# Optimization experiments

Measured on AMD Instinct MI355X. Metric: run time of the kernel, lower is better.

## Reference

```python
import jax, jax.numpy as jnp
import numpy as np

B, T, M = 4, 512, 77
H, D = 10, 64            # num_heads, latent_dim
LAT = H * D              # 640 = latent_dim * num_heads
E, TOPK, FFN = 8, 2, 256 # experts, top-k, 4*latent_dim
TED = 512                # time_embed_dim
NDS = 4                  # num_datasets


def layernorm(x, g, b, eps=1e-5):
    m = x.mean(-1, keepdims=True)
    v = ((x - m) ** 2).mean(-1, keepdims=True)
    return (x - m) * jax.lax.rsqrt(v + eps) * g + b


def moe_ffn(x, wg, w1, b1, w2, b2):
    # x: (N, D). Top-k gated mixture of expert FFNs (tutel-style, fp32 gate,
    # no capacity truncation in this reference).
    logits = x.astype(jnp.float32) @ wg.astype(jnp.float32)        # (N, E)
    scores = jax.nn.softmax(logits, -1)
    vals, idx = jax.lax.top_k(scores, TOPK)                        # (N, k)
    comb = (jax.nn.one_hot(idx, E, dtype=scores.dtype) * vals[..., None]).sum(1)  # (N, E)
    h = jax.nn.gelu(jnp.einsum('nd,edf->nef', x, w1) + b1)         # (N, E, F)
    y = jnp.einsum('nef,efd->ned', h, w2) + b2                     # (N, E, D)
    return jnp.einsum('ne,ned->nd', comb.astype(x.dtype), y)


def setup_inputs() -> dict:
    key = jax.random.key(0)
    ks = jax.random.split(key, 24)
    s = 0.02
    f32 = jnp.float32
    return {
        'x': jax.random.normal(ks[0], (B, T, LAT), f32),
        'emb': jax.random.normal(ks[1], (B, T, TED), f32),
        'src_mask': jax.random.randint(ks[2], (B, T), 0, 2).astype(jnp.int32),
        'motion_length': jax.random.randint(ks[3], (B,), 1, T).astype(jnp.int32),
        'num_intervals': 1,
        'text_cond': jnp.ones((B, 1), f32),
        'text_word_out': jax.random.normal(ks[4], (B, M, LAT), f32),
        'norm_g': jnp.ones((LAT,), f32), 'norm_b': jnp.zeros((LAT,), f32),
        'moe_emb': jax.random.normal(ks[5], (1, T, H, D), f32) * s,
        'm_wg': jax.random.normal(ks[6], (D, E), f32) * s,
        'm_w1': jax.random.normal(ks[7], (E, D, FFN), f32) * s,
        'm_b1': jnp.zeros((E, FFN), f32),
        'm_w2': jax.random.normal(ks[8], (E, FFN, D), f32) * s,
        'm_b2': jnp.zeros((E, D), f32),
        'm_proj_w': jax.random.normal(ks[9], (D, 5 * D), f32) * s,
        'm_proj_b': jnp.zeros((5 * D,), f32),
        'key_motion_scale': jnp.ones((), f32),
        'sigma': jnp.asarray(100.0, f32),
        'key_dataset': jax.random.normal(ks[10], (NDS, 48, H, D), f32) * s,
        'key_dataset_scale': jnp.ones((), f32),
        'value_dataset': jax.random.normal(ks[11], (NDS, 48, H, D), f32) * s,
        'key_rotation': jax.random.normal(ks[12], (3, 16, H, D), f32) * s,
        'key_rotation_scale': jnp.ones((), f32),
        'value_rotation': jax.random.normal(ks[13], (3, 16, H, D), f32) * s,
        'normt_g': jnp.ones((LAT,), f32), 'normt_b': jnp.zeros((LAT,), f32),
        'c_wg': jax.random.normal(ks[14], (D, E), f32) * s,
        'c_w1': jax.random.normal(ks[15], (E, D, FFN), f32) * s,
        'c_b1': jnp.zeros((E, FFN), f32),
        'c_w2': jax.random.normal(ks[16], (E, FFN, D), f32) * s,
        'c_b2': jnp.zeros((E, D), f32),
        'c_proj_w': jax.random.normal(ks[17], (D, 2 * D), f32) * s,
        'c_proj_b': jnp.zeros((2 * D,), f32),
        'key_text_scale': jnp.ones((), f32),
        'st_emb_w': jax.random.normal(ks[18], (TED, 2 * LAT), f32) * s,
        'st_emb_b': jnp.zeros((2 * LAT,), f32),
        'st_norm_g': jnp.ones((LAT,), f32), 'st_norm_b': jnp.zeros((LAT,), f32),
        'st_out_w': jax.random.normal(ks[19], (LAT, LAT), f32) * s,
        'st_out_b': jnp.zeros((LAT,), f32),
    }


def reference(x, emb, src_mask, motion_length, num_intervals, text_cond, text_word_out,
              norm_g, norm_b, moe_emb, m_wg, m_w1, m_b1, m_w2, m_b2, m_proj_w, m_proj_b,
              key_motion_scale, sigma, key_dataset, key_dataset_scale, value_dataset,
              key_rotation, key_rotation_scale, value_rotation, normt_g, normt_b,
              c_wg, c_w1, c_b1, c_w2, c_b2, c_proj_w, c_proj_b, key_text_scale,
              st_emb_w, st_emb_b, st_norm_g, st_norm_b, st_out_w, st_out_b):
    b, t, _ = x.shape
    # motion MoE -> per-head q, k, v (output is 5*D; last 2 chunks are template feats, unused here)
    xh = layernorm(x, norm_g, norm_b).reshape(b, t, H, D) + moe_emb[:, :t]
    y = moe_ffn(xh.reshape(-1, D), m_wg, m_w1, m_b1, m_w2, m_b2)
    y = (jax.nn.gelu(y) @ m_proj_w + m_proj_b).reshape(b, t, H, 5 * D)
    q, k_m, v_m = y[..., :D], y[..., D:2 * D], y[..., 2 * D:3 * D]

    # text conditioning MoE -> key/value (output is 2*D)
    m = text_word_out.shape[1]
    ct = layernorm(text_word_out, normt_g, normt_b).reshape(b, m, H, D)
    cy = moe_ffn(ct.reshape(-1, D), c_wg, c_w1, c_b1, c_w2, c_b2)
    cy = (jax.nn.gelu(cy) @ c_proj_w + c_proj_b).reshape(b, m, H, 2 * D)
    k_t, v_t = cy[..., :D], cy[..., D:]

    sc = D ** -0.5
    # motion keys: Gaussian time-locality bias (sigma) + src_mask
    lg_m = jnp.einsum('bthd,bshd->bhts', q, k_m * key_motion_scale) * sc
    ti = jnp.arange(t)
    lg_m = lg_m - ((ti[:, None] - ti[None, :]).astype(x.dtype) ** 2) / (2.0 * sigma ** 2)
    lg_m = jnp.where((src_mask > 0)[:, None, None, :], lg_m, -1e9)
    # dataset / rotation learned key-value banks (dataset index 0)
    lg_d = jnp.einsum('bthd,shd->bhts', q, key_dataset[0] * key_dataset_scale) * sc
    lg_r = jnp.einsum('bthd,shd->bhts', q, key_rotation.reshape(-1, H, D) * key_rotation_scale) * sc
    # text keys, masked by text_cond
    lg_t = jnp.einsum('bthd,bmhd->bhtm', q, k_t * key_text_scale) * sc
    lg_t = jnp.where((text_cond[:, 0] > 0)[:, None, None, None], lg_t, -1e9)

    attn = jax.nn.softmax(jnp.concatenate([lg_m, lg_d, lg_r, lg_t], -1), -1)
    a_m, a_d = attn[..., :t], attn[..., t:t + 48]
    a_r, a_t = attn[..., t + 48:t + 96], attn[..., t + 96:]
    out = (jnp.einsum('bhts,bshd->bthd', a_m, v_m)
           + jnp.einsum('bhts,shd->bthd', a_d, value_dataset[0])
           + jnp.einsum('bhts,shd->bthd', a_r, value_rotation.reshape(-1, H, D))
           + jnp.einsum('bhtm,bmhd->bthd', a_t, v_t)).reshape(b, t, LAT)

    # StylizationBlock (MotionDiffuse-style) + residual
    eo = jax.nn.silu(emb) @ st_emb_w + st_emb_b            # (B,T,2*LAT)
    hh = layernorm(out, st_norm_g, st_norm_b) * (1.0 + eo[..., :LAT]) + eo[..., LAT:]
    return x + (jax.nn.silu(hh) @ st_out_w + st_out_b)
```

## Files before the change

kernel.cpp:

```cpp
#include <hip/hip_runtime.h>
#include <math.h>

#define BB 4
#define TT 512
#define MM 77
#define HH 10
#define DD 64
#define LATD 640
#define EE 8
#define FFND 256
#define NS 685
#define NCH 11
#define NROWS 20480
#define NSPLIT 4

#define NTOK_M (BB*TT*HH)
#define NTOK_T (BB*MM*HH)
#define MAXB_M 647
#define MAXB_T 103
#define PROJB_M 320
#define PROJB_T 49
#define ROUTEB_M 80
#define ROUTEB_T 13
#define ATTNB (BB*HH*8*NSPLIT)
#define GEMM1B 1280

typedef float f32x4 __attribute__((ext_vector_type(4)));
typedef __bf16 bf16x8_t __attribute__((ext_vector_type(8)));
typedef unsigned short u16x8 __attribute__((ext_vector_type(8)));

__device__ __forceinline__ float geluf(float x){
    float u = 0.7978845608028654f*(x + 0.044715f*x*x*x);
    u = fminf(fmaxf(u, -15.f), 15.f);
    float e = __expf(2.f*u);
    return 0.5f*x*(1.f + (e-1.f)/(e+1.f));
}
__device__ __forceinline__ float siluf(float x){
    return x / (1.0f + __expf(-x));
}
__device__ __forceinline__ unsigned short f2bf(float f){
    unsigned int u = __float_as_uint(f);
    u += 0x7fff + ((u >> 16) & 1);
    return (unsigned short)(u >> 16);
}
__device__ __forceinline__ uint2 pack4bf(float a, float b, float c, float d){
    uint2 r;
    r.x = (unsigned)f2bf(a) | ((unsigned)f2bf(b)<<16);
    r.y = (unsigned)f2bf(c) | ((unsigned)f2bf(d)<<16);
    return r;
}

__global__ __launch_bounds__(256) void prep_ln_kernel(
    const float* __restrict__ m_w1, unsigned short* __restrict__ w1Tm,
    const float* __restrict__ m_w2, unsigned short* __restrict__ w2Tm,
    const float* __restrict__ c_w1, unsigned short* __restrict__ w1Tt,
    const float* __restrict__ c_w2, unsigned short* __restrict__ w2Tt,
    const float* __restrict__ st_ew, unsigned short* __restrict__ stewT,
    const float* __restrict__ st_ow, unsigned short* __restrict__ stowT,
    const float* __restrict__ m_pw, unsigned short* __restrict__ mpwT,
    const float* __restrict__ c_pw, unsigned short* __restrict__ cpwT,
    const float* __restrict__ emb, unsigned short* __restrict__ embBf,
    int* __restrict__ cnt,
    const float* __restrict__ x, const float* __restrict__ ng, const float* __restrict__ nb,
    const float* __restrict__ memb, float* __restrict__ xh,
    const float* __restrict__ two, const float* __restrict__ ntg, const float* __restrict__ ntb,
    float* __restrict__ ctB)
{
    __shared__ float buf[64*65];
    const int bid = blockIdx.x, tid = threadIdx.x;
    if (bid >= 651){
        int lrow = bid - 651;
        const float* in; const float* g; const float* bb; const float* ap; float* out;
        int row;
        if (lrow < BB*TT){
            row = lrow; in = x; g = ng; bb = nb; out = xh;
            ap = memb + (size_t)(row % TT)*LATD;
        } else {
            row = lrow - BB*TT; in = two; g = ntg; bb = ntb; out = ctB;
            ap = nullptr;
        }
        float* xsr = buf;
        float* red = buf + LATD;
        const float* rp = in + (size_t)row*LATD;
        float s = 0.f;
        for (int i=tid;i<LATD;i+=256){ float v = rp[i]; xsr[i]=v; s+=v; }
        red[tid]=s; __syncthreads();
        for (int k=128;k>0;k>>=1){ if (tid<k) red[tid]+=red[tid+k]; __syncthreads(); }
        float mean = red[0]*(1.0f/LATD);
        __syncthreads();
        float vs=0.f;
        for (int i=tid;i<LATD;i+=256){ float d=xsr[i]-mean; vs+=d*d; }
        red[tid]=vs; __syncthreads();
        for (int k=128;k>0;k>>=1){ if (tid<k) red[tid]+=red[tid+k]; __syncthreads(); }
        float rstd = rsqrtf(red[0]*(1.0f/LATD)+1e-5f);
        float* op = out + (size_t)row*LATD;
        for (int i=tid;i<LATD;i+=256){
            float v = (xsr[i]-mean)*rstd*g[i] + bb[i];
            if (ap) v += ap[i];
            op[i] = v;
        }
        return;
    }
    if (bid >= 395){
        int l = bid - 395;
        if (l == 0 && tid < 16) cnt[tid] = 0;
        size_t base = (size_t)l*4096;
        #pragma unroll
        for (int p=0; p<4; ++p){
            size_t i = base + (size_t)p*1024 + tid*4;
            float4 v = *(const float4*)(emb + i);
            *(uint2*)(embBf + i) = pack4bf(siluf(v.x), siluf(v.y), siluf(v.z), siluf(v.w));
        }
        return;
    }
    float (*t)[65] = (float(*)[65])buf;
    const float* in; unsigned short* out; int R, C, z, rt, ct;
    if (bid < 32)      { int l=bid;     in=m_w1;  out=w1Tm;  R=64;  C=256;  z=l>>2; rt=0;    ct=l&3; }
    else if (bid < 64) { int l=bid-32;  in=m_w2;  out=w2Tm;  R=256; C=64;   z=l>>2; rt=l&3;  ct=0; }
    else if (bid < 96) { int l=bid-64;  in=c_w1;  out=w1Tt;  R=64;  C=256;  z=l>>2; rt=0;    ct=l&3; }
    else if (bid < 128){ int l=bid-96;  in=c_w2;  out=w2Tt;  R=256; C=64;   z=l>>2; rt=l&3;  ct=0; }
    else if (bid < 288){ int l=bid-128; in=st_ew; out=stewT; R=512; C=1280; z=0;    rt=l/20; ct=l%20; }
    else if (bid < 388){ int l=bid-288; in=st_ow; out=stowT; R=640; C=640;  z=0;    rt=l/10; ct=l%10; }
    else if (bid < 393){ int l=bid-388; in=m_pw;  out=mpwT;  R=64;  C=320;  z=0;    rt=0;    ct=l; }
    else               { int l=bid-393; in=c_pw;  out=cpwT;  R=64;  C=128;  z=0;    rt=0;    ct=l; }
    const size_t base = (size_t)z*R*C;
    const int r0 = rt*64, c0 = ct*64;
    #pragma unroll
    for (int p=0; p<16; ++p){
        int i = tid + p*256;
        int r = i>>6, c = i&63;
        t[r][c] = in[base + (size_t)(r0+r)*C + c0 + c];
    }
    __syncthreads();
    #pragma unroll
    for (int p=0; p<16; ++p){
        int i = tid + p*256;
        int c = i>>6, r = i&63;
        out[base + (size_t)(c0+c)*R + r0 + r] = f2bf(t[r][c]);
    }
}

__global__ __launch_bounds__(256) void route_kernel(
    const float* __restrict__ xinM, const float* __restrict__ wgM,
    int* __restrict__ countsM, int* __restrict__ listM, float* __restrict__ wAM,
    const float* __restrict__ xinT, const float* __restrict__ wgT,
    int* __restrict__ countsT, int* __restrict__ listT, float* __restrict__ wAT)
{
    __shared__ int bcnt[EE];
    __shared__ int bbase[EE];
    const int tid = threadIdx.x;
    const int bid = blockIdx.x;
    const float* xin; const float* wg; int* counts; int* list; float* wA; int nTok, t;
    if (bid < ROUTEB_M){
        xin = xinM; wg = wgM; counts = countsM; list = listM; wA = wAM; nTok = NTOK_M;
        t = bid*256 + tid;
    } else {
        xin = xinT; wg = wgT; counts = countsT; list = listT; wA = wAT; nTok = NTOK_T;
        t = (bid - ROUTEB_M)*256 + tid;
    }
    if (tid < EE) bcnt[tid] = 0;
    __syncthreads();

    int e0 = 0, e1 = 0, p0 = 0, p1 = 0;
    bool act = (t < nTok);
    if (act){
        float lg[EE];
        #pragma unroll
        for (int e=0;e<EE;e++) lg[e]=0.f;
        const float4* xp = (const float4*)(xin + (size_t)t*DD);
        #pragma unroll 4
        for (int dq=0; dq<16; ++dq){
            float4 xv = xp[dq];
            const float* w0 = wg + (dq*4+0)*EE;
            const float* w1 = wg + (dq*4+1)*EE;
            const float* w2 = wg + (dq*4+2)*EE;
            const float* w3 = wg + (dq*4+3)*EE;
            #pragma unroll
            for (int e=0;e<EE;e++)
                lg[e] += xv.x*w0[e] + xv.y*w1[e] + xv.z*w2[e] + xv.w*w3[e];
        }
        float mx = lg[0];
        #pragma unroll
        for (int e=1;e<EE;e++) mx = fmaxf(mx, lg[e]);
        float sum = 0.f;
        #pragma unroll
        for (int e=0;e<EE;e++){ lg[e] = __expf(lg[e]-mx); sum += lg[e]; }
        float inv = 1.0f/sum;
        #pragma unroll
        for (int e=0;e<EE;e++) lg[e] *= inv;
        float v0=lg[0];
        #pragma unroll
        for (int e=1;e<EE;e++){ if (lg[e] > v0){ v0 = lg[e]; e0 = e; } }
        float v1=-1e30f; e1 = (e0==0) ? 1 : 0;
        #pragma unroll
        for (int e=0;e<EE;e++){ if (e==e0) continue; if (lg[e] > v1){ v1 = lg[e]; e1 = e; } }
        wA[t*2+0]=v0; wA[t*2+1]=v1;
        p0 = atomicAdd(&bcnt[e0], 1);
        p1 = atomicAdd(&bcnt[e1], 1);
    }
    __syncthreads();
    if (tid < EE){
        bbase[tid] = (bcnt[tid] > 0) ? atomicAdd(&counts[tid], bcnt[tid]) : 0;
    }
    __syncthreads();
    if (act){
        list[(size_t)e0*nTok + bbase[e0] + p0] = t*2;
        list[(size_t)e1*nTok + bbase[e1] + p1] = t*2+1;
    }
}

__global__ __launch_bounds__(256) void moe_ffn_kernel(
    const float* __restrict__ xinM, const unsigned short* __restrict__ w1TM,
    const float* __restrict__ b1M, const unsigned short* __restrict__ w2TM,
    const float* __restrict__ b2M, const int* __restrict__ countsM,
    const int* __restrict__ listM, const float* __restrict__ wAM,
    float* __restrict__ yslotM,
    const float* __restrict__ xinT, const unsigned short* __restrict__ w1TT,
    const float* __restrict__ b1T, const unsigned short* __restrict__ w2TT,
    const float* __restrict__ b2T, const int* __restrict__ countsT,
    const int* __restrict__ listT, const float* __restrict__ wAT,
    float* __restrict__ yslotT)
{
    __shared__ __align__(16) unsigned short xs[64][72];
    __shared__ __align__(16) unsigned short w1s[64][72];
    __shared__ __align__(16) unsigned short w2s[64][72];
    __shared__ __align__(16) unsigned short hs[64][72];
    __shared__ int sCnt[EE];
    __shared__ int encs[64];
    __shared__ float wgts[64];
    const int tid = threadIdx.x;
    const float* xin; const unsigned short* w1T; const float* b1g;
    const unsigned short* w2T; const float* b2g; const int* counts;
    const int* list; const float* wA; float* yslot; int nTok, bidl;
    if (blockIdx.x < MAXB_M){
        xin=xinM; w1T=w1TM; b1g=b1M; w2T=w2TM; b2g=b2M; counts=countsM;
        list=listM; wA=wAM; yslot=yslotM; nTok=NTOK_M; bidl=blockIdx.x;
    } else {
        xin=xinT; w1T=w1TT; b1g=b1T; w2T=w2TT; b2g=b2T; counts=countsT;
        list=listT; wA=wAT; yslot=yslotT; nTok=NTOK_T; bidl=blockIdx.x-MAXB_M;
    }
    if (tid < EE) sCnt[tid] = counts[tid];
    __syncthreads();
    int e = -1, tile = 0;
    {
        int acc = 0;
        #pragma unroll
        for (int i=0;i<EE;++i){
            int tc = (sCnt[i]+63)>>6;
            if (e < 0 && bidl < acc + tc){ e = i; tile = bidl - acc; }
            acc += tc;
        }
    }
    if (e < 0) return;
    const int cnt = sCnt[e];
    if (tid < 64){
        int idx = tile*64 + tid;
        int enc = (idx < cnt) ? list[(size_t)e*nTok + idx] : -1;
        encs[tid] = enc;
        wgts[tid] = (enc >= 0) ? wA[enc] : 0.f;
    }
    __syncthreads();
    for (int i=tid; i<64*16; i+=256){
        int r = i>>4, dq4 = (i&15)*4;
        int enc = encs[r];
        float4 xv = make_float4(0.f,0.f,0.f,0.f);
        if (enc >= 0) xv = *(const float4*)(xin + (size_t)(enc>>1)*DD + dq4);
        *(uint2*)&xs[r][dq4] = pack4bf(xv.x, xv.y, xv.z, xv.w);
    }

    const int w    = tid >> 6;
    const int lane = tid & 63;
    const int lq   = lane & 15;
    const int lg   = lane >> 4;

    const unsigned short* w1e = w1T + (size_t)e*FFND*DD;
    const unsigned short* w2e = w2T + (size_t)e*DD*FFND;

    f32x4 acc2[4] = {};

    for (int fc=0; fc<4; ++fc){
        __syncthreads();
        for (int i=tid; i<512; i+=256){
            int r = i>>3, jq = i&7;
            *(uint4*)&w1s[r][jq*8] = *(const uint4*)(w1e + (size_t)(fc*64+r)*DD + jq*8);
            *(uint4*)&w2s[r][jq*8] = *(const uint4*)(w2e + (size_t)r*FFND + fc*64 + jq*8);
        }
        __syncthreads();
        f32x4 acc1[4] = {};
        #pragma unroll
        for (int fb=0; fb<4; ++fb){
            #pragma unroll
            for (int ks=0; ks<2; ++ks){
                bf16x8_t xf = *reinterpret_cast<const bf16x8_t*>(&xs[w*16+lq][ks*32+lg*8]);
                bf16x8_t wf = *reinterpret_cast<const bf16x8_t*>(&w1s[fb*16+lq][ks*32+lg*8]);
                acc1[fb] = __builtin_amdgcn_mfma_f32_16x16x32_bf16(xf, wf, acc1[fb], 0, 0, 0);
            }
        }
        #pragma unroll
        for (int fb=0; fb<4; ++fb){
            float b1v = b1g[e*FFND + fc*64 + fb*16 + lq];
            #pragma unroll
            for (int r=0; r<4; ++r)
                hs[w*16 + lg*4 + r][fb*16 + lq] = f2bf(geluf(acc1[fb][r] + b1v));
        }
        #pragma unroll
        for (int db=0; db<4; ++db){
            #pragma unroll
            for (int ks=0; ks<2; ++ks){
                bf16x8_t hf  = *reinterpret_cast<const bf16x8_t*>(&hs[w*16+lq][ks*32+lg*8]);
                bf16x8_t w2f = *reinterpret_cast<const bf16x8_t*>(&w2s[db*16+lq][ks*32+lg*8]);
                acc2[db] = __builtin_amdgcn_mfma_f32_16x16x32_bf16(hf, w2f, acc2[db], 0, 0, 0);
            }
        }
    }
    #pragma unroll
    for (int r=0; r<4; ++r){
        int tok = w*16 + lg*4 + r;
        int enc = encs[tok];
        if (enc >= 0){
            float gw = wgts[tok];
            #pragma unroll
            for (int db=0; db<4; ++db){
                int d = db*16 + lq;
                yslot[(size_t)enc*DD + d] = gw*(acc2[db][r] + b2g[e*DD + d]);
            }
        }
    }
}

template<int NPROJ>
__device__ __forceinline__ void proj_body(
    const float* __restrict__ yslot, const unsigned short* __restrict__ pwT,
    const float* __restrict__ pbg, int nTok, int base,
    float* __restrict__ out0, float* __restrict__ out1, float* __restrict__ out2,
    unsigned short gs[64][72])
{
    const int tid = threadIdx.x;
    for (int i=tid; i<64*16; i+=256){
        int r = i>>4, dq4 = (i&15)*4;
        int tok = base + r;
        float4 g4 = make_float4(0.f,0.f,0.f,0.f);
        if (tok < nTok){
            float4 a = *(const float4*)(yslot + (size_t)tok*128 + dq4);
            float4 b = *(const float4*)(yslot + (size_t)tok*128 + 64 + dq4);
            g4.x = geluf(a.x+b.x); g4.y = geluf(a.y+b.y);
            g4.z = geluf(a.z+b.z); g4.w = geluf(a.w+b.w);
        }
        *(uint2*)&gs[r][dq4] = pack4bf(g4.x, g4.y, g4.z, g4.w);
    }
    __syncthreads();

    const int w    = tid >> 6;
    const int lane = tid & 63;
    const int lq   = lane & 15;
    const int lg   = lane >> 4;
    constexpr int NC = NPROJ/64;
    const int colbase = w*16*NC;

    bf16x8_t wf[NC][2];
    #pragma unroll
    for (int cb=0; cb<NC; ++cb)
        #pragma unroll
        for (int ks=0; ks<2; ++ks)
            wf[cb][ks] = *reinterpret_cast<const bf16x8_t*>(
                pwT + (size_t)(colbase + cb*16 + lq)*DD + ks*32 + lg*8);

    f32x4 acc[4][NC] = {};
    #pragma unroll
    for (int m=0; m<4; ++m){
        #pragma unroll
        for (int ks=0; ks<2; ++ks){
            bf16x8_t af = *reinterpret_cast<const bf16x8_t*>(&gs[m*16+lq][ks*32+lg*8]);
            #pragma unroll
            for (int cb=0; cb<NC; ++cb)
                acc[m][cb] = __builtin_amdgcn_mfma_f32_16x16x32_bf16(af, wf[cb][ks], acc[m][cb], 0, 0, 0);
        }
    }
    #pragma unroll
    for (int m=0; m<4; ++m){
        #pragma unroll
        for (int r=0; r<4; ++r){
            int tok = base + m*16 + lg*4 + r;
            if (tok >= nTok) continue;
            #pragma unroll
            for (int cb=0; cb<NC; ++cb){
                int j = colbase + cb*16 + lq;
                float v = acc[m][cb][r] + pbg[j];
                int bufi = j >> 6, jd = j & 63;
                float* dst = (bufi==0) ? out0 : (bufi==1) ? out1 : out2;
                dst[(size_t)tok*DD + jd] = v;
            }
        }
    }
}

__global__ __launch_bounds__(256) void moe_proj_kernel(
    const float* __restrict__ yslotM, const unsigned short* __restrict__ mpwT,
    const float* __restrict__ mpb,
    float* __restrict__ qB, float* __restrict__ kmB, float* __restrict__ vmB,
    const float* __restrict__ yslotT, const unsigned short* __restrict__ cpwT,
    const float* __restrict__ cpb,
    float* __restrict__ ktB, float* __restrict__ vtB)
{
    __shared__ __align__(16) unsigned short gs[64][72];
    if (blockIdx.x < PROJB_M){
        proj_body<192>(yslotM, mpwT, mpb, NTOK_M, blockIdx.x*64, qB, kmB, vmB, gs);
    } else {
        proj_body<128>(yslotT, cpwT, cpb, NTOK_T, (blockIdx.x-PROJB_M)*64, ktB, vtB, nullptr, gs);
    }
}

__global__ __launch_bounds__(256) void attn_gemm_kernel(
    const float* __restrict__ qb,
    const float* __restrict__ kmb,
    const float* __restrict__ vmb,
    const float* __restrict__ ktb,
    const float* __restrict__ vtb,
    const float* __restrict__ kd,
    const float* __restrict__ vd,
    const float* __restrict__ kr,
    const float* __restrict__ vr,
    const int*   __restrict__ smask,
    const float* __restrict__ tcond,
    const float* __restrict__ kms_p, const float* __restrict__ kds_p,
    const float* __restrict__ krs_p, const float* __restrict__ kts_p,
    const float* __restrict__ sigma_p,
    float* __restrict__ po, float* __restrict__ pm, float* __restrict__ pl,
    const unsigned short* __restrict__ gA,
    const unsigned short* __restrict__ gWt,
    const float* __restrict__ gbias, float* __restrict__ gC)
{
    __shared__ __align__(16) unsigned char smem[27904];
    const int tid  = threadIdx.x;

    if (blockIdx.x >= ATTNB){
        const int gbid = blockIdx.x - ATTNB;
        unsigned short (*As)[40] = (unsigned short(*)[40])smem;
        unsigned short (*Bs)[40] = (unsigned short(*)[40])(smem + 2560);
        const int Nr = 1280, Kr = 512;
        const int row0 = (gbid & 63)*32, col0 = (gbid >> 6)*64;
        const int wave = tid >> 6, lane = tid & 63;
        const int lr = lane & 15, lk = lane >> 4;
        f32x4 acc[2] = {};
        for (int k0 = 0; k0 < Kr; k0 += 32){
            __syncthreads();
            {
                int r = tid >> 3, kq = tid & 7;
                *(uint2*)&As[r][kq*4] = *(const uint2*)(gA + (size_t)(row0 + r)*Kr + k0 + kq*4);
            }
            {
                int n = tid >> 2, oq = tid & 3;
                *(uint4*)&Bs[n][oq*8] = *(const uint4*)(gWt + (size_t)(col0+n)*Kr + k0 + oq*8);
            }
            __syncthreads();
            bf16x8_t a0 = *reinterpret_cast<const bf16x8_t*>(&As[lr][lk*8]);
            bf16x8_t a1 = *reinterpret_cast<const bf16x8_t*>(&As[16 + lr][lk*8]);
            bf16x8_t bfr = *reinterpret_cast<const bf16x8_t*>(&Bs[wave*16 + lr][lk*8]);
            acc[0] = __builtin_amdgcn_mfma_f32_16x16x32_bf16(a0, bfr, acc[0], 0, 0, 0);
            acc[1] = __builtin_amdgcn_mfma_f32_16x16x32_bf16(a1, bfr, acc[1], 0, 0, 0);
        }
        int gc = col0 + wave*16 + lr;
        float bv = gbias[gc];
        #pragma unroll
        for (int m=0;m<2;++m){
            #pragma unroll
            for (int r=0;r<4;++r){
                int gr = row0 + m*16 + lk*4 + r;
                gC[(size_t)gr*Nr + gc] = acc[m][r] + bv;
            }
        }
        return;
    }

    unsigned short (*Ks)[72] = (unsigned short(*)[72])smem;
    unsigned short (*Vt)[72] = (unsigned short(*)[72])(smem + 9216);
    unsigned short (*Pl)[72] = (unsigned short(*)[72])(smem + 18432);
    float* madd = (float*)(smem + 27648);

    const int w    = tid >> 6;
    const int lane = tid & 63;
    const int lq   = lane & 15;
    const int lg   = lane >> 4;

    const int split = blockIdx.x & 3;
    const int xb    = blockIdx.x >> 2;
    const int ch_lo = split*3;
    const int ch_hi = min(ch_lo + 3, NCH);
    const int ttile = xb & 7;
    const int bh    = xb >> 3;
    const int b = bh / HH, h = bh % HH;
    const int t0 = ttile * 64;

    const float sc = 0.125f;
    const float kms = kms_p[0]*sc, kds = kds_p[0]*sc, krs = krs_p[0]*sc, kts = kts_p[0]*sc;
    const float sg = sigma_p[0];
    const float inv2s = 1.0f/(2.0f*sg*sg);
    const bool text_on = tcond[b] > 0.f;

    bf16x8_t qf[2];
    {
        const float* qrow = qb + ((size_t)(b*TT + t0 + w*16 + lq)*HH + h)*DD;
        #pragma unroll
        for (int ks=0; ks<2; ++ks){
            float4 v0 = *(const float4*)(qrow + ks*32 + lg*8);
            float4 v1 = *(const float4*)(qrow + ks*32 + lg*8 + 4);
            u16x8 qt;
            qt[0]=f2bf(v0.x); qt[1]=f2bf(v0.y); qt[2]=f2bf(v0.z); qt[3]=f2bf(v0.w);
            qt[4]=f2bf(v1.x); qt[5]=f2bf(v1.y); qt[6]=f2bf(v1.z); qt[7]=f2bf(v1.w);
            qf[ks] = __builtin_bit_cast(bf16x8_t, qt);
        }
    }

    float m_r = -1e30f, l_r = 0.f;
    f32x4 oacc[4] = {};

    const int tgq = t0 + w*16 + lq;

    for (int ch=ch_lo; ch<ch_hi; ++ch){
        __syncthreads();
        for (int i=tid; i<64*16; i+=256){
            int r = i>>4, dq4 = (i&15)*4;
            int s = ch*64 + r;
            float4 kv = make_float4(0,0,0,0), vv = make_float4(0,0,0,0);
            if (s < TT){
                size_t o = ((size_t)(b*TT + s)*HH + h)*DD + dq4;
                kv = *(const float4*)(&kmb[o]);
                kv.x*=kms; kv.y*=kms; kv.z*=kms; kv.w*=kms;
                vv = *(const float4*)(&vmb[o]);
            } else if (s < TT+48){
                kv = *(const float4*)(&kd[((size_t)(s-TT)*HH + h)*DD + dq4]);
                kv.x*=kds; kv.y*=kds; kv.z*=kds; kv.w*=kds;
                vv = *(const float4*)(&vd[((size_t)(s-TT)*HH + h)*DD + dq4]);
            } else if (s < TT+96){
                kv = *(const float4*)(&kr[((size_t)(s-TT-48)*HH + h)*DD + dq4]);
                kv.x*=krs; kv.y*=krs; kv.z*=krs; kv.w*=krs;
                vv = *(const float4*)(&vr[((size_t)(s-TT-48)*HH + h)*DD + dq4]);
            } else if (s < NS){
                size_t o = ((size_t)(b*MM + (s-TT-96))*HH + h)*DD + dq4;
                kv = *(const float4*)(&ktb[o]);
                kv.x*=kts; kv.y*=kts; kv.z*=kts; kv.w*=kts;
                vv = *(const float4*)(&vtb[o]);
            }
            *(uint2*)&Ks[r][dq4] = pack4bf(kv.x, kv.y, kv.z, kv.w);
            int swcol = r ^ (((i&15)&7)<<3);
            Vt[dq4+0][swcol] = f2bf(vv.x);
            Vt[dq4+1][swcol] = f2bf(vv.y);
            Vt[dq4+2][swcol] = f2bf(vv.z);
            Vt[dq4+3][swcol] = f2bf(vv.w);
        }
        if (tid < 64){
            int s = ch*64 + tid;
            float a;
            if (s < TT)            a = (smask[b*TT + s] == 0) ? -1e9f : 0.f;
            else if (s < TT+96)    a = 0.f;
            else if (s < NS)       a = text_on ? 0.f : -1e9f;
            else                   a = -1e30f;
            madd[tid] = a;
        }
        __syncthreads();

        f32x4 sacc[4] = {};
        #pragma unroll
        for (int sl=0; sl<4; ++sl){
            #pragma unroll
            for (int ks=0; ks<2; ++ks){
                bf16x8_t kf = *reinterpret_cast<const bf16x8_t*>(&Ks[sl*16 + lq][ks*32 + lg*8]);
                sacc[sl] = __builtin_amdgcn_mfma_f32_16x16x32_bf16(kf, qf[ks], sacc[sl], 0, 0, 0);
            }
        }
        float sv[4][4];
        float pmax = -1e30f;
        #pragma unroll
        for (int sl=0; sl<4; ++sl){
            #pragma unroll
            for (int r=0; r<4; ++r){
                int s_loc = sl*16 + lg*4 + r;
                float a = madd[s_loc];
                if (ch < 8){ float dt = (float)(tgq - (ch*64 + s_loc)); a -= dt*dt*inv2s; }
                float v = sacc[sl][r] + a;
                sv[sl][r] = v;
                pmax = fmaxf(pmax, v);
            }
        }
        pmax = fmaxf(pmax, __shfl_xor(pmax, 16));
        pmax = fmaxf(pmax, __shfl_xor(pmax, 32));
        float mn  = fmaxf(m_r, pmax);
        float scl = __expf(m_r - mn);
        m_r = mn;
        float psum = 0.f;
        #pragma unroll
        for (int sl=0; sl<4; ++sl){
            #pragma unroll
            for (int r=0; r<4; ++r){
                float p = __expf(sv[sl][r] - mn);
                sv[sl][r] = p;
                psum += p;
            }
        }
        psum += __shfl_xor(psum, 16);
        psum += __shfl_xor(psum, 32);
        l_r = l_r*scl + psum;
        #pragma unroll
        for (int sl=0; sl<4; ++sl)
            *(uint2*)&Pl[w*16 + lq][sl*16 + lg*4] = pack4bf(sv[sl][0], sv[sl][1], sv[sl][2], sv[sl][3]);

        #pragma unroll
        for (int r=0; r<4; ++r){
            float so = __shfl(scl, lg*4 + r);
            #pragma unroll
            for (int ds_=0; ds_<4; ++ds_) oacc[ds_][r] *= so;
        }
        #pragma unroll
        for (int ds_=0; ds_<4; ++ds_){
            int dcol = ds_*16 + lq;
            int swz = (((dcol>>2)&7)<<3);
            #pragma unroll
            for (int ks=0; ks<2; ++ks){
                bf16x8_t pf = *reinterpret_cast<const bf16x8_t*>(&Pl[w*16 + lq][ks*32 + lg*8]);
                bf16x8_t vf = *reinterpret_cast<const bf16x8_t*>(&Vt[dcol][(ks*32 + lg*8) ^ swz]);
                oacc[ds_] = __builtin_amdgcn_mfma_f32_16x16x32_bf16(pf, vf, oacc[ds_], 0, 0, 0);
            }
        }
    }
    #pragma unroll
    for (int r=0; r<4; ++r){
        int t = t0 + w*16 + lg*4 + r;
        size_t off = (size_t)split*NROWS + (size_t)bh*TT + t;
        #pragma unroll
        for (int ds_=0; ds_<4; ++ds_)
            po[off*64 + ds_*16 + lq] = oacc[ds_][r];
    }
    if (lg == 0){
        size_t off = (size_t)split*NROWS + (size_t)bh*TT + (t0 + w*16 + lq);
        pm[off] = m_r;
        pl[off] = l_r;
    }
}

__global__ __launch_bounds__(256) void gemm_mfma_kernel(
    const float* __restrict__ A, const unsigned short* __restrict__ Wt,
    const float* __restrict__ bias, const float* __restrict__ res,
    float* __restrict__ C, int Mr, int Nr, int Kr)
{
    __shared__ __align__(16) unsigned short As[32][40];
    __shared__ __align__(16) unsigned short Bs[64][40];
    int tid = threadIdx.x;
    int row0 = blockIdx.x*32, col0 = blockIdx.y*64;
    int wave = tid >> 6, lane = tid & 63;
    int lr = lane & 15, lk = lane >> 4;

    f32x4 acc[2] = {};

    for (int k0 = 0; k0 < Kr; k0 += 32){
        __syncthreads();
        {
            int r = tid >> 3, kq = tid & 7;
            float4 v = *(const float4*)(A + (size_t)(row0 + r)*Kr + k0 + kq*4);
            *(uint2*)&As[r][kq*4] = pack4bf(v.x, v.y, v.z, v.w);
        }
        {
            int n = tid >> 2, oq = tid & 3;
            *(uint4*)&Bs[n][oq*8] = *(const uint4*)(Wt + (size_t)(col0+n)*Kr + k0 + oq*8);
        }
        __syncthreads();
        bf16x8_t a0 = *reinterpret_cast<const bf16x8_t*>(&As[lr][lk*8]);
        bf16x8_t a1 = *reinterpret_cast<const bf16x8_t*>(&As[16 + lr][lk*8]);
        bf16x8_t bfr = *reinterpret_cast<const bf16x8_t*>(&Bs[wave*16 + lr][lk*8]);
        acc[0] = __builtin_amdgcn_mfma_f32_16x16x32_bf16(a0, bfr, acc[0], 0, 0, 0);
        acc[1] = __builtin_amdgcn_mfma_f32_16x16x32_bf16(a1, bfr, acc[1], 0, 0, 0);
    }
    int gc = col0 + wave*16 + lr;
    float bv = bias[gc];
    #pragma unroll
    for (int m=0;m<2;++m){
        #pragma unroll
        for (int r=0;r<4;++r){
            int gr = row0 + m*16 + lk*4 + r;
            float v = acc[m][r] + bv;
            size_t off = (size_t)gr*Nr + gc;
            if (res) v += res[off];
            C[off] = v;
        }
    }
}

__global__ __launch_bounds__(256) void lnmod_combine_kernel(
    const float* __restrict__ po, const float* __restrict__ pm, const float* __restrict__ pl,
    const float* __restrict__ g, const float* __restrict__ bb,
    const float* __restrict__ eo, float* __restrict__ out)
{
    int row = blockIdx.x, tid = threadIdx.x;
    int b = row / TT, t = row % TT;
    __shared__ float xsr[LATD];
    __shared__ float red[256];
    float s = 0.f;
    for (int i=tid;i<LATD;i+=256){
        int h = i >> 6, d = i & 63;
        size_t rowid = ((size_t)(b*HH + h))*TT + t;
        float m = -1e30f;
        #pragma unroll
        for (int k=0;k<NSPLIT;++k) m = fmaxf(m, pm[(size_t)k*NROWS + rowid]);
        float lsum = 0.f, acc = 0.f;
        #pragma unroll
        for (int k=0;k<NSPLIT;++k){
            float sk = __expf(pm[(size_t)k*NROWS + rowid] - m);
            lsum += pl[(size_t)k*NROWS + rowid]*sk;
            acc  += po[((size_t)k*NROWS + rowid)*64 + d]*sk;
        }
        float v = acc / lsum;
        xsr[i] = v; s += v;
    }
    red[tid]=s; __syncthreads();
    for (int k=128;k>0;k>>=1){ if (tid<k) red[tid]+=red[tid+k]; __syncthreads(); }
    float mean = red[0]*(1.0f/LATD);
    __syncthreads();
    float vs=0.f;
    for (int i=tid;i<LATD;i+=256){ float d=xsr[i]-mean; vs+=d*d; }
    red[tid]=vs; __syncthreads();
    for (int k=128;k>0;k>>=1){ if (tid<k) red[tid]+=red[tid+k]; __syncthreads(); }
    float rstd = rsqrtf(red[0]*(1.0f/LATD)+1e-5f);
    const float* ep = eo + (size_t)row*(2*LATD);
    float* op = out + (size_t)row*LATD;
    for (int i=tid;i<LATD;i+=256){
        float v = (xsr[i]-mean)*rstd*g[i] + bb[i];
        v = v*(1.0f + ep[i]) + ep[LATD+i];
        op[i] = siluf(v);
    }
}

extern "C" void kernel_launch(void* const* d_in, const int* in_sizes, int n_in,
                              void* d_out, int out_size, void* d_ws, size_t ws_size,
                              hipStream_t stream)
{
    (void)in_sizes; (void)n_in; (void)out_size; (void)ws_size;
    const float* x     = (const float*)d_in[0];
    const float* emb   = (const float*)d_in[1];
    const int*   smask = (const int*)d_in[2];
    const float* tcond = (const float*)d_in[5];
    const float* two   = (const float*)d_in[6];
    const float* ng    = (const float*)d_in[7];
    const float* nb    = (const float*)d_in[8];
    const float* memb  = (const float*)d_in[9];
    const float* m_wg  = (const float*)d_in[10];
    const float* m_w1  = (const float*)d_in[11];
    const float* m_b1  = (const float*)d_in[12];
    const float* m_w2  = (const float*)d_in[13];
    const float* m_b2  = (const float*)d_in[14];
    const float* m_pw  = (const float*)d_in[15];
    const float* m_pb  = (const float*)d_in[16];
    const float* kms   = (const float*)d_in[17];
    const float* sigma = (const float*)d_in[18];
    const float* kdat  = (const float*)d_in[19];
    const float* kds   = (const float*)d_in[20];
    const float* vdat  = (const float*)d_in[21];
    const float* krot  = (const float*)d_in[22];
    const float* krs   = (const float*)d_in[23];
    const float* vrot  = (const float*)d_in[24];
    const float* ntg   = (const float*)d_in[25];
    const float* ntb   = (const float*)d_in[26];
    const float* c_wg  = (const float*)d_in[27];
    const float* c_w1  = (const float*)d_in[28];
    const float* c_b1  = (const float*)d_in[29];
    const float* c_w2  = (const float*)d_in[30];
    const float* c_b2  = (const float*)d_in[31];
    const float* c_pw  = (const float*)d_in[32];
    const float* c_pb  = (const float*)d_in[33];
    const float* kts   = (const float*)d_in[34];
    const float* st_ew = (const float*)d_in[35];
    const float* st_eb = (const float*)d_in[36];
    const float* st_ng = (const float*)d_in[37];
    const float* st_nb = (const float*)d_in[38];
    const float* st_ow = (const float*)d_in[39];
    const float* st_ob = (const float*)d_in[40];

    float* ws = (float*)d_ws;
    float* xh   = ws;
    float* qB   = xh  + 1310720;
    float* kmB  = qB  + 1310720;
    float* vmB  = kmB + 1310720;
    float* ctB  = vmB + 1310720;
    float* ktB  = ctB + 197120;
    float* vtB  = ktB + 197120;
    float* aout = vtB + 197120;
    float* eoB  = aout + 1310720;
    float* shB  = eoB + 2621440;

    unsigned short* w1Tm = (unsigned short*)(shB + 1310720);
    unsigned short* w2Tm = w1Tm + EE*FFND*DD;
    unsigned short* w1Tt = w2Tm + EE*FFND*DD;
    unsigned short* w2Tt = w1Tt + EE*FFND*DD;
    unsigned short* stewT = w2Tt + EE*FFND*DD;
    unsigned short* stowT = stewT + 512*1280;
    unsigned short* mpwT  = stowT + 640*640;
    unsigned short* cpwT  = mpwT + 320*64;
    unsigned short* embBf = cpwT + 128*64;
    float* poB = (float*)(embBf + 2048*512);
    float* pmB = poB + (size_t)NSPLIT*NROWS*64;
    float* plB = pmB + (size_t)NSPLIT*NROWS;

    float* yslotM = eoB;
    float* yslotT = shB;
    float* wAm   = aout;
    float* wAt   = wAm + NTOK_M*2;
    int*   cntA  = (int*)(wAt + NTOK_T*2);
    int*   listM = cntA + 16;
    int*   listT = listM + EE*NTOK_M;

    prep_ln_kernel<<<651 + BB*TT + BB*MM, 256, 0, stream>>>(
        m_w1, w1Tm, m_w2, w2Tm, c_w1, w1Tt, c_w2, w2Tt,
        st_ew, stewT, st_ow, stowT, m_pw, mpwT, c_pw, cpwT,
        emb, embBf, cntA,
        x, ng, nb, memb, xh, two, ntg, ntb, ctB);

    route_kernel<<<ROUTEB_M + ROUTEB_T, 256, 0, stream>>>(
        xh, m_wg, cntA, listM, wAm,
        ctB, c_wg, cntA+8, listT, wAt);

    moe_ffn_kernel<<<MAXB_M + MAXB_T, 256, 0, stream>>>(
        xh, w1Tm, m_b1, w2Tm, m_b2, cntA, listM, wAm, yslotM,
        ctB, w1Tt, c_b1, w2Tt, c_b2, cntA+8, listT, wAt, yslotT);

    moe_proj_kernel<<<PROJB_M + PROJB_T, 256, 0, stream>>>(
        yslotM, mpwT, m_pb, qB, kmB, vmB,
        yslotT, cpwT, c_pb, ktB, vtB);

    attn_gemm_kernel<<<ATTNB + GEMM1B, 256, 0, stream>>>(
        qB, kmB, vmB, ktB, vtB, kdat, vdat, krot, vrot, smask, tcond,
        kms, kds, krs, kts, sigma, poB, pmB, plB,
        embBf, stewT, st_eb, eoB);

    lnmod_combine_kernel<<<BB*TT, 256, 0, stream>>>(
        poB, pmB, plB, st_ng, st_nb, eoB, shB);

    {
        dim3 g2(2048/32, 640/64);
        gemm_mfma_kernel<<<g2, 256, 0, stream>>>(shB, stowT, st_ob, x, (float*)d_out, 2048, 640, 640);
    }
}
```

Before: 112.6 us.

## Precompute bf16 K/V chunks and mask once; emit bf16 activations for final GEMM

Adds a kv_prep kernel that converts, scales and transposes the motion, dataset, rotation and text K/V into per-(batch,head,chunk) bf16 tiles plus a mask array. The attention kernel then loads them with plain 16-byte copies instead of redoing fp32 loads and conversion in each of the 8 time tiles. lnmod_combine now writes bf16, so the output GEMM loads bf16 directly. The cost is an extra launch and extra workspace traffic.

```diff
diff --git a/kernel.cpp b/kernel.cpp
--- a/kernel.cpp
+++ b/kernel.cpp
@@ -11,6 +11,7 @@
 #define FFND 256
 #define NS 685
 #define NCH 11
+#define NSP (NCH*64)
 #define NROWS 20480
 #define NSPLIT 4
 
@@ -410,20 +411,77 @@
     }
 }
 
+__global__ __launch_bounds__(256) void kv_prep_kernel(
+    const float* __restrict__ kmb, const float* __restrict__ vmb,
+    const float* __restrict__ ktb, const float* __restrict__ vtb,
+    const float* __restrict__ kd,  const float* __restrict__ vd,
+    const float* __restrict__ kr,  const float* __restrict__ vr,
+    const int*   __restrict__ smask, const float* __restrict__ tcond,
+    const float* __restrict__ kms_p, const float* __restrict__ kds_p,
+    const float* __restrict__ krs_p, const float* __restrict__ kts_p,
+    unsigned short* __restrict__ Kbf,
+    unsigned short* __restrict__ VTbf,
+    float* __restrict__ maddg)
+{
+    __shared__ __align__(16) unsigned short Vs[64][72];
+    const int tid = threadIdx.x;
+    const int bh = blockIdx.x, ch = blockIdx.y;
+    const int b = bh / HH, h = bh % HH;
+    const float sc = 0.125f;
+    const float kms = kms_p[0]*sc, kds = kds_p[0]*sc, krs = krs_p[0]*sc, kts = kts_p[0]*sc;
+    unsigned short* kc = Kbf + ((size_t)(bh*NCH + ch) << 12);
+    unsigned short* vc = VTbf + ((size_t)(bh*NCH + ch) << 12);
+    for (int i=tid; i<64*16; i+=256){
+        int r = i>>4, dq4 = (i&15)*4;
+        int s = ch*64 + r;
+        float4 kv = make_float4(0,0,0,0), vv = make_float4(0,0,0,0);
+        if (s < TT){
+            size_t o = ((size_t)(b*TT + s)*HH + h)*DD + dq4;
+            kv = *(const float4*)(&kmb[o]);
+            kv.x*=kms; kv.y*=kms; kv.z*=kms; kv.w*=kms;
+            vv = *(const float4*)(&vmb[o]);
+        } else if (s < TT+48){
+            kv = *(const float4*)(&kd[((size_t)(s-TT)*HH + h)*DD + dq4]);
+            kv.x*=kds; kv.y*=kds; kv.z*=kds; kv.w*=kds;
+            vv = *(const float4*)(&vd[((size_t)(s-TT)*HH + h)*DD + dq4]);
+        } else if (s < TT+96){
+            kv = *(const float4*)(&kr[((size_t)(s-TT-48)*HH + h)*DD + dq4]);
+            kv.x*=krs; kv.y*=krs; kv.z*=krs; kv.w*=krs;
+            vv = *(const float4*)(&vr[((size_t)(s-TT-48)*HH + h)*DD + dq4]);
+        } else if (s < NS){
+            size_t o = ((size_t)(b*MM + (s-TT-96))*HH + h)*DD + dq4;
+            kv = *(const float4*)(&ktb[o]);
+            kv.x*=kts; kv.y*=kts; kv.z*=kts; kv.w*=kts;
+            vv = *(const float4*)(&vtb[o]);
+        }
+        *(uint2*)(kc + r*64 + dq4) = pack4bf(kv.x, kv.y, kv.z, kv.w);
+        int swcol = r ^ (((i&15)&7)<<3);
+        Vs[dq4+0][swcol] = f2bf(vv.x);
+        Vs[dq4+1][swcol] = f2bf(vv.y);
+        Vs[dq4+2][swcol] = f2bf(vv.z);
+        Vs[dq4+3][swcol] = f2bf(vv.w);
+    }
+    __syncthreads();
+    for (int i=tid; i<512; i+=256){
+        int d = i>>3, seg = i&7;
+        *(uint4*)(vc + d*64 + seg*8) = *(const uint4*)&Vs[d][seg*8];
+    }
+    if (h == 0 && tid < 64){
+        int s = ch*64 + tid;
+        float a;
+        if (s < TT)            a = (smask[b*TT + s] == 0) ? -1e9f : 0.f;
+        else if (s < TT+96)    a = 0.f;
+        else if (s < NS)       a = (tcond[b] > 0.f) ? 0.f : -1e9f;
+        else                   a = -1e30f;
+        maddg[b*NSP + s] = a;
+    }
+}
+
 __global__ __launch_bounds__(256) void attn_gemm_kernel(
     const float* __restrict__ qb,
-    const float* __restrict__ kmb,
-    const float* __restrict__ vmb,
-    const float* __restrict__ ktb,
-    const float* __restrict__ vtb,
-    const float* __restrict__ kd,
-    const float* __restrict__ vd,
-    const float* __restrict__ kr,
-    const float* __restrict__ vr,
-    const int*   __restrict__ smask,
-    const float* __restrict__ tcond,
-    const float* __restrict__ kms_p, const float* __restrict__ kds_p,
-    const float* __restrict__ krs_p, const float* __restrict__ kts_p,
+    const unsigned short* __restrict__ Kbf,
+    const unsigned short* __restrict__ VTbf,
+    const float* __restrict__ maddg,
     const float* __restrict__ sigma_p,
     float* __restrict__ po, float* __restrict__ pm, float* __restrict__ pl,
     const unsigned short* __restrict__ gA,
@@ -491,11 +549,8 @@
     const int b = bh / HH, h = bh % HH;
     const int t0 = ttile * 64;
 
-    const float sc = 0.125f;
-    const float kms = kms_p[0]*sc, kds = kds_p[0]*sc, krs = krs_p[0]*sc, kts = kts_p[0]*sc;
     const float sg = sigma_p[0];
     const float inv2s = 1.0f/(2.0f*sg*sg);
-    const bool text_on = tcond[b] > 0.f;
 
     bf16x8_t qf[2];
     {
@@ -515,47 +570,24 @@
     f32x4 oacc[4] = {};
 
     const int tgq = t0 + w*16 + lq;
+    const float* mrow = maddg + b*NSP;
 
     for (int ch=ch_lo; ch<ch_hi; ++ch){
         __syncthreads();
-        for (int i=tid; i<64*16; i+=256){
-            int r = i>>4, dq4 = (i&15)*4;
-            int s = ch*64 + r;
-            float4 kv = make_float4(0,0,0,0), vv = make_float4(0,0,0,0);
-            if (s < TT){
-                size_t o = ((size_t)(b*TT + s)*HH + h)*DD + dq4;
-                kv = *(const float4*)(&kmb[o]);
-                kv.x*=kms; kv.y*=kms; kv.z*=kms; kv.w*=kms;
-                vv = *(const float4*)(&vmb[o]);
-            } else if (s < TT+48){
-                kv = *(const float4*)(&kd[((size_t)(s-TT)*HH + h)*DD + dq4]);
-                kv.x*=kds; kv.y*=kds; kv.z*=kds; kv.w*=kds;
-                vv = *(const float4*)(&vd[((size_t)(s-TT)*HH + h)*DD + dq4]);
-            } else if (s < TT+96){
-                kv = *(const float4*)(&kr[((size_t)(s-TT-48)*HH + h)*DD + dq4]);
-                kv.x*=krs; kv.y*=krs; kv.z*=krs; kv.w*=krs;
-                vv = *(const float4*)(&vr[((size_t)(s-TT-48)*HH + h)*DD + dq4]);
-            } else if (s < NS){
-                size_t o = ((size_t)(b*MM + (s-TT-96))*HH + h)*DD + dq4;
-                kv = *(const float4*)(&ktb[o]);
-                kv.x*=kts; kv.y*=kts; kv.z*=kts; kv.w*=kts;
-                vv = *(const float4*)(&vtb[o]);
-            }
-            *(uint2*)&Ks[r][dq4] = pack4bf(kv.x, kv.y, kv.z, kv.w);
-            int swcol = r ^ (((i&15)&7)<<3);
-            Vt[dq4+0][swcol] = f2bf(vv.x);
-            Vt[dq4+1][swcol] = f2bf(vv.y);
-            Vt[dq4+2][swcol] = f2bf(vv.z);
-            Vt[dq4+3][swcol] = f2bf(vv.w);
-        }
-        if (tid < 64){
-            int s = ch*64 + tid;
-            float a;
-            if (s < TT)            a = (smask[b*TT + s] == 0) ? -1e9f : 0.f;
-            else if (s < TT+96)    a = 0.f;
-            else if (s < NS)       a = text_on ? 0.f : -1e9f;
-            else                   a = -1e30f;
-            madd[tid] = a;
+        {
+            const unsigned short* kc = Kbf + ((size_t)(bh*NCH + ch) << 12);
+            const unsigned short* vc = VTbf + ((size_t)(bh*NCH + ch) << 12);
+            #pragma unroll
+            for (int p=0; p<4; ++p){
+                int i = tid + p*256;
+                int bsel = i >> 9, j = i & 511;
+                int r = j >> 3, seg = j & 7;
+                if (bsel == 0)
+                    *(uint4*)&Ks[r][seg*8] = *(const uint4*)(kc + r*64 + seg*8);
+                else
+                    *(uint4*)&Vt[r][seg*8] = *(const uint4*)(vc + r*64 + seg*8);
+            }
+            if (tid < 64) madd[tid] = mrow[ch*64 + tid];
         }
         __syncthreads();
 
@@ -638,7 +670,7 @@
 }
 
 __global__ __launch_bounds__(256) void gemm_mfma_kernel(
-    const float* __restrict__ A, const unsigned short* __restrict__ Wt,
+    const unsigned short* __restrict__ A, const unsigned short* __restrict__ Wt,
     const float* __restrict__ bias, const float* __restrict__ res,
     float* __restrict__ C, int Mr, int Nr, int Kr)
 {
@@ -655,8 +687,7 @@
         __syncthreads();
         {
             int r = tid >> 3, kq = tid & 7;
-            float4 v = *(const float4*)(A + (size_t)(row0 + r)*Kr + k0 + kq*4);
-            *(uint2*)&As[r][kq*4] = pack4bf(v.x, v.y, v.z, v.w);
+            *(uint2*)&As[r][kq*4] = *(const uint2*)(A + (size_t)(row0 + r)*Kr + k0 + kq*4);
         }
         {
             int n = tid >> 2, oq = tid & 3;
@@ -687,7 +718,7 @@
 __global__ __launch_bounds__(256) void lnmod_combine_kernel(
     const float* __restrict__ po, const float* __restrict__ pm, const float* __restrict__ pl,
     const float* __restrict__ g, const float* __restrict__ bb,
-    const float* __restrict__ eo, float* __restrict__ out)
+    const float* __restrict__ eo, unsigned short* __restrict__ outBf)
 {
     int row = blockIdx.x, tid = threadIdx.x;
     int b = row / TT, t = row % TT;
@@ -720,11 +751,11 @@
     for (int k=128;k>0;k>>=1){ if (tid<k) red[tid]+=red[tid+k]; __syncthreads(); }
     float rstd = rsqrtf(red[0]*(1.0f/LATD)+1e-5f);
     const float* ep = eo + (size_t)row*(2*LATD);
-    float* op = out + (size_t)row*LATD;
+    unsigned short* op = outBf + (size_t)row*LATD;
     for (int i=tid;i<LATD;i+=256){
         float v = (xsr[i]-mean)*rstd*g[i] + bb[i];
         v = v*(1.0f + ep[i]) + ep[LATD+i];
-        op[i] = siluf(v);
+        op[i] = f2bf(siluf(v));
     }
 }
 
@@ -797,9 +828,13 @@
     float* poB = (float*)(embBf + 2048*512);
     float* pmB = poB + (size_t)NSPLIT*NROWS*64;
     float* plB = pmB + (size_t)NSPLIT*NROWS;
+    unsigned short* KbfB  = (unsigned short*)(plB + (size_t)NSPLIT*NROWS);
+    unsigned short* VTbfB = KbfB + (size_t)BB*HH*NCH*4096;
+    float* maddB = (float*)(VTbfB + (size_t)BB*HH*NCH*4096);
 
     float* yslotM = eoB;
     float* yslotT = shB;
+    unsigned short* shBf = (unsigned short*)shB;
     float* wAm   = aout;
     float* wAt   = wAm + NTOK_M*2;
     int*   cntA  = (int*)(wAt + NTOK_T*2);
@@ -824,16 +859,22 @@
         yslotM, mpwT, m_pb, qB, kmB, vmB,
         yslotT, cpwT, c_pb, ktB, vtB);
 
+    {
+        dim3 gp(BB*HH, NCH);
+        kv_prep_kernel<<<gp, 256, 0, stream>>>(
+            kmB, vmB, ktB, vtB, kdat, vdat, krot, vrot, smask, tcond,
+            kms, kds, krs, kts, KbfB, VTbfB, maddB);
+    }
+
     attn_gemm_kernel<<<ATTNB + GEMM1B, 256, 0, stream>>>(
-        qB, kmB, vmB, ktB, vtB, kdat, vdat, krot, vrot, smask, tcond,
-        kms, kds, krs, kts, sigma, poB, pmB, plB,
+        qB, KbfB, VTbfB, maddB, sigma, poB, pmB, plB,
         embBf, stewT, st_eb, eoB);
 
     lnmod_combine_kernel<<<BB*TT, 256, 0, stream>>>(
-        poB, pmB, plB, st_ng, st_nb, eoB, shB);
+        poB, pmB, plB, st_ng, st_nb, eoB, shBf);
 
     {
         dim3 g2(2048/32, 640/64);
-        gemm_mfma_kernel<<<g2, 256, 0, stream>>>(shB, stowT, st_ob, x, (float*)d_out, 2048, 640, 640);
-    }
-}
+        gemm_mfma_kernel<<<g2, 256, 0, stream>>>(shBf, stowT, st_ob, x, (float*)d_out, 2048, 640, 640);
+    }
+}
```

New measurement: 111.2 us, median of 2. Within noise of the previous version (-1.2%).
